# Kernel tuning notes

Measured on AMD Instinct MI355X. Metric: run time of the kernel, lower is better.

Reference implementation:

```python
import jax, jax.numpy as jnp
import numpy as np

EPS = 1e-8  # torch F.cosine_similarity eps


def setup_inputs() -> dict:
    key = jax.random.key(0)
    k1, k2 = jax.random.split(key)
    B, D = 8192, 512
    return {
        "label_tensor": jnp.arange(B, dtype=jnp.int64),
        "feature_a": jax.random.normal(k1, (B, D), dtype=jnp.float32),
        "feature_b": jax.random.normal(k2, (B, D), dtype=jnp.float32),
        "affine_w": jnp.ones((1,), dtype=jnp.float32),   # AffineModel scale
        "affine_b": jnp.zeros((1,), dtype=jnp.float32),  # AffineModel bias
    }


def reference(label_tensor, feature_a, feature_b, affine_w, affine_b):
    # cos_score[i, j] = cos(a_i, b_j): normalize then one [B,D]x[D,B] GEMM
    a_n = feature_a / jnp.maximum(
        jnp.linalg.norm(feature_a, axis=1, keepdims=True), EPS)
    b_n = feature_b / jnp.maximum(
        jnp.linalg.norm(feature_b, axis=1, keepdims=True), EPS)
    cos_score = jnp.einsum("id,jd->ij", a_n, b_n)  # [B, B]
    cos_score = affine_w[0] * cos_score + affine_b[0]  # AffineModel
    # cross-entropy with labels = arange(B) -> diagonal of log_softmax
    logp = jax.nn.log_softmax(cos_score, axis=1)
    B = cos_score.shape[0]
    loss = -jnp.mean(logp[jnp.arange(B), jnp.arange(B)])
    return (loss, cos_score)
```

## Files before the change

### kernel.cpp

```cpp
#include <hip/hip_runtime.h>
#include <hip/hip_bf16.h>

#define B_ROWS 8192
#define DIM 512

typedef __bf16 bf16x8 __attribute__((ext_vector_type(8)));
typedef float f32x4 __attribute__((ext_vector_type(4)));

__device__ inline ushort f2bf(float x) {
    __hip_bfloat16 h = __float2bfloat16(x);
    return __builtin_bit_cast(ushort, h);
}

__global__ __launch_bounds__(256) void norm_kernel(const float* __restrict__ A,
                                                   const float* __restrict__ Bf,
                                                   ushort* __restrict__ An,
                                                   ushort* __restrict__ Bn) {
    int gw = (blockIdx.x * 256 + threadIdx.x) >> 6;
    int lane = threadIdx.x & 63;
    const float* src;
    ushort* dst;
    if (gw < B_ROWS) {
        src = A + (size_t)gw * DIM;
        dst = An + (size_t)gw * DIM;
    } else {
        src = Bf + (size_t)(gw - B_ROWS) * DIM;
        dst = Bn + (size_t)(gw - B_ROWS) * DIM;
    }
    const float4* s4 = (const float4*)src;
    float4 v0 = s4[lane * 2];
    float4 v1 = s4[lane * 2 + 1];
    float ss = v0.x * v0.x + v0.y * v0.y + v0.z * v0.z + v0.w * v0.w
             + v1.x * v1.x + v1.y * v1.y + v1.z * v1.z + v1.w * v1.w;
#pragma unroll
    for (int m = 32; m >= 1; m >>= 1) ss += __shfl_xor(ss, m, 64);
    float scale = 1.0f / fmaxf(sqrtf(ss), 1e-8f);
    union { ushort us[8]; uint4 q; } o;
    o.us[0] = f2bf(v0.x * scale); o.us[1] = f2bf(v0.y * scale);
    o.us[2] = f2bf(v0.z * scale); o.us[3] = f2bf(v0.w * scale);
    o.us[4] = f2bf(v1.x * scale); o.us[5] = f2bf(v1.y * scale);
    o.us[6] = f2bf(v1.z * scale); o.us[7] = f2bf(v1.w * scale);
    ((uint4*)dst)[lane] = o.q;
}

#define GLDS(src, dst) __builtin_amdgcn_global_load_lds( \
    (const __attribute__((address_space(1))) unsigned int*)(src), \
    (__attribute__((address_space(3))) unsigned int*)(dst), 16, 0, 0)

__global__ __launch_bounds__(512, 2) void gemm_kernel(
    const ushort* __restrict__ An, const ushort* __restrict__ Bn,
    float* __restrict__ C, float* __restrict__ rowpart,
    const float* __restrict__ wp, const float* __restrict__ bp) {
    __shared__ ushort ldsA[2][8192];
    __shared__ ushort ldsB[2][8192];

    const int t = threadIdx.x;
    const int brow = blockIdx.y * 256;
    const int bcol = blockIdx.x * 256;
    const int wid = t >> 6, lane = t & 63;
    const int wr = wid >> 2, wc = wid & 3;
    const int fr = lane & 15;
    const int fhi = lane >> 4;

    const int srow = t >> 2;
    const int schunk = (t & 3) ^ ((t >> 3) & 3);
    const ushort* gA0 = An + (size_t)(brow + srow) * DIM + schunk * 8;
    const ushort* gA1 = gA0 + (size_t)128 * DIM;
    const ushort* gB0 = Bn + (size_t)(bcol + srow) * DIM + schunk * 8;
    const ushort* gB1 = gB0 + (size_t)128 * DIM;

#define STAGE(buf, kt) do { const int k0_ = (kt) * 32;            \
        GLDS(gA0 + k0_, &ldsA[buf][t * 8]);                       \
        GLDS(gA1 + k0_, &ldsA[buf][4096 + t * 8]);                \
        GLDS(gB0 + k0_, &ldsB[buf][t * 8]);                       \
        GLDS(gB1 + k0_, &ldsB[buf][4096 + t * 8]); } while (0)

    f32x4 acc[8][4];
#pragma unroll
    for (int i = 0; i < 8; i++)
#pragma unroll
        for (int j = 0; j < 4; j++) acc[i][j] = (f32x4){0.f, 0.f, 0.f, 0.f};

    const int rchunk = (fhi ^ ((fr >> 1) & 3)) * 8;

    STAGE(0, 0);
    __syncthreads();

    int cur = 0;
#pragma unroll
    for (int kt = 0; kt < 16; ++kt) {
        if (kt < 15) STAGE(cur ^ 1, kt + 1);
        bf16x8 af[8], bfr[4];
#pragma unroll
        for (int m = 0; m < 8; ++m)
            af[m] = *(const bf16x8*)&ldsA[cur][(wr * 128 + m * 16 + fr) * 32 + rchunk];
#pragma unroll
        for (int n = 0; n < 4; ++n)
            bfr[n] = *(const bf16x8*)&ldsB[cur][(wc * 64 + n * 16 + fr) * 32 + rchunk];
        __builtin_amdgcn_s_setprio(1);
#pragma unroll
        for (int m = 0; m < 8; ++m)
#pragma unroll
            for (int n = 0; n < 4; ++n)
                acc[m][n] = __builtin_amdgcn_mfma_f32_16x16x32_bf16(af[m], bfr[n], acc[m][n], 0, 0, 0);
        __builtin_amdgcn_s_setprio(0);
        __syncthreads();
        cur ^= 1;
    }

    const float w = wp[0], bb = bp[0];
    const float M = fabsf(w) + fabsf(bb);
    float* part = (float*)&ldsA[0][0];
#pragma unroll
    for (int m = 0; m < 8; ++m) {
#pragma unroll
        for (int r = 0; r < 4; ++r) {
            const int rloc = wr * 128 + m * 16 + fhi * 4 + r;
            const size_t grow = (size_t)(brow + rloc);
            float psum = 0.f;
#pragma unroll
            for (int n = 0; n < 4; ++n) {
                const int gcol = bcol + wc * 64 + n * 16 + fr;
                float s = fmaf(w, acc[m][n][r], bb);
                C[grow * B_ROWS + gcol] = s;
                psum += __expf(s - M);
            }
#pragma unroll
            for (int msk = 1; msk <= 8; msk <<= 1) psum += __shfl_xor(psum, msk, 64);
            if (fr == 0) part[wc * 256 + rloc] = psum;
        }
    }
    __syncthreads();
    if (t < 256) {
        float s = part[t] + part[256 + t] + part[512 + t] + part[768 + t];
        rowpart[(size_t)blockIdx.x * B_ROWS + brow + t] = s;
    }
#undef STAGE
}

__global__ __launch_bounds__(256) void loss_kernel(const float* __restrict__ C,
                                                   const float* __restrict__ rowpart,
                                                   const float* __restrict__ wp,
                                                   const float* __restrict__ bp,
                                                   float* __restrict__ out0) {
    __shared__ float sred[4];
    const int row = blockIdx.x * 256 + threadIdx.x;
    float rs = 0.f;
#pragma unroll
    for (int j = 0; j < 32; ++j) rs += rowpart[(size_t)j * B_ROWS + row];
    const float M = fabsf(wp[0]) + fabsf(bp[0]);
    const float sii = C[(size_t)row * B_ROWS + row];
    float v = sii - M - __logf(rs);
#pragma unroll
    for (int msk = 32; msk >= 1; msk >>= 1) v += __shfl_xor(v, msk, 64);
    if ((threadIdx.x & 63) == 0) sred[threadIdx.x >> 6] = v;
    __syncthreads();
    if (threadIdx.x == 0) {
        float tot = sred[0] + sred[1] + sred[2] + sred[3];
        atomicAdd(out0, -tot / (float)B_ROWS);
    }
}

extern "C" void kernel_launch(void* const* d_in, const int* in_sizes, int n_in,
                              void* d_out, int out_size, void* d_ws, size_t ws_size,
                              hipStream_t stream) {
    const float* A  = (const float*)d_in[1];
    const float* Bf = (const float*)d_in[2];
    const float* wp = (const float*)d_in[3];
    const float* bp = (const float*)d_in[4];
    float* out = (float*)d_out;

    ushort* An = (ushort*)d_ws;
    ushort* Bn = An + (size_t)B_ROWS * DIM;
    float* rowpart = (float*)((char*)d_ws + (size_t)2 * B_ROWS * DIM * sizeof(ushort));

    hipMemsetAsync(d_out, 0, sizeof(float), stream);
    norm_kernel<<<dim3(16384 * 64 / 256), 256, 0, stream>>>(A, Bf, An, Bn);
    dim3 grid(B_ROWS / 256, B_ROWS / 256);
    gemm_kernel<<<grid, 512, 0, stream>>>(An, Bn, out + 1, rowpart, wp, bp);
    loss_kernel<<<B_ROWS / 256, 256, 0, stream>>>(out + 1, rowpart, wp, bp, out);
}
```

Before: 397.7 us.

## Restructure GEMM main loop into K=64 steps with interleaved staging and MFMA quadrants

The GEMM kernel now stages a K=64 slice per iteration (8 iterations instead of 16) and splits each iteration into four MFMA quadrants. Global-to-LDS loads for A and B halves are interleaved between quadrants under explicit s_waitcnt vmcnt and s_barrier control. The aim is to overlap memory staging with tensor-core work and halve the per-K-step barrier count. In exchange it doubles LDS use to 128 KB per block, which may cut occupancy below the two blocks per CU requested by the launch bounds. The hand-placed barriers and vmcnt counts also risk subtle ordering errors.

Result: faster. 387.7 us (-2.5%).

```diff
diff --git a/kernel.cpp b/kernel.cpp
--- a/kernel.cpp
+++ b/kernel.cpp
@@ -47,12 +47,18 @@
     (const __attribute__((address_space(1))) unsigned int*)(src), \
     (__attribute__((address_space(3))) unsigned int*)(dst), 16, 0, 0)
 
+#define STG(bufv, ab, PTR, doff, ktv) do {                                   \
+    GLDS((PTR) + (ktv) * 64,      L + (((bufv)*2 + (ab))*2 + 0)*8192 + (doff)); \
+    GLDS((PTR) + (ktv) * 64 + 32, L + (((bufv)*2 + (ab))*2 + 1)*8192 + (doff)); } while (0)
+
+#define BARRIER() asm volatile("s_barrier" ::: "memory")
+
 __global__ __launch_bounds__(512, 2) void gemm_kernel(
     const ushort* __restrict__ An, const ushort* __restrict__ Bn,
     float* __restrict__ C, float* __restrict__ rowpart,
     const float* __restrict__ wp, const float* __restrict__ bp) {
-    __shared__ ushort ldsA[2][8192];
-    __shared__ ushort ldsB[2][8192];
+    __shared__ ushort lds[2][2][2][8192];
+    ushort* L = &lds[0][0][0][0];
 
     const int t = threadIdx.x;
     const int brow = blockIdx.y * 256;
@@ -62,18 +68,19 @@
     const int fr = lane & 15;
     const int fhi = lane >> 4;
 
-    const int srow = t >> 2;
-    const int schunk = (t & 3) ^ ((t >> 3) & 3);
-    const ushort* gA0 = An + (size_t)(brow + srow) * DIM + schunk * 8;
-    const ushort* gA1 = gA0 + (size_t)128 * DIM;
-    const ushort* gB0 = Bn + (size_t)(bcol + srow) * DIM + schunk * 8;
-    const ushort* gB1 = gB0 + (size_t)128 * DIM;
-
-#define STAGE(buf, kt) do { const int k0_ = (kt) * 32;            \
-        GLDS(gA0 + k0_, &ldsA[buf][t * 8]);                       \
-        GLDS(gA1 + k0_, &ldsA[buf][4096 + t * 8]);                \
-        GLDS(gB0 + k0_, &ldsB[buf][t * 8]);                       \
-        GLDS(gB1 + k0_, &ldsB[buf][4096 + t * 8]); } while (0)
+    const int schunk8 = ((t & 3) ^ ((t >> 3) & 3)) * 8;
+    const int srowAa = (t >> 8) * 128 + ((t >> 2) & 63);
+    const int srowBa = (t >> 7) * 64 + ((t >> 2) & 31);
+    const ushort* pAa = An + (size_t)(brow + srowAa) * DIM + schunk8;
+    const ushort* pAb = An + (size_t)(brow + srowAa + 64) * DIM + schunk8;
+    const ushort* pBa = Bn + (size_t)(bcol + srowBa) * DIM + schunk8;
+    const ushort* pBb = Bn + (size_t)(bcol + srowBa + 32) * DIM + schunk8;
+    const int dAa = t * 8 + (t >> 8) * 2048;
+    const int dAb = dAa + 2048;
+    const int dBa = t * 8 + (t >> 7) * 1024;
+    const int dBb = dBa + 1024;
+
+    const int rchunk8 = (fhi ^ ((fr >> 1) & 3)) * 8;
 
     f32x4 acc[8][4];
 #pragma unroll
@@ -81,36 +88,76 @@
 #pragma unroll
         for (int j = 0; j < 4; j++) acc[i][j] = (f32x4){0.f, 0.f, 0.f, 0.f};
 
-    const int rchunk = (fhi ^ ((fr >> 1) & 3)) * 8;
-
-    STAGE(0, 0);
+    bf16x8 af[4][2], b0[2][2], b1[2][2];
+
+    auto rdA = [&](int buf, int mb) {
+#pragma unroll
+        for (int i = 0; i < 4; ++i)
+#pragma unroll
+            for (int kk = 0; kk < 2; ++kk)
+                af[i][kk] = *(const bf16x8*)(L + ((buf * 2 + 0) * 2 + kk) * 8192
+                            + (wr * 128 + (mb + i) * 16 + fr) * 32 + rchunk8);
+    };
+    auto rdB = [&](bf16x8 (&b)[2][2], int buf, int nb) {
+#pragma unroll
+        for (int j = 0; j < 2; ++j)
+#pragma unroll
+            for (int kk = 0; kk < 2; ++kk)
+                b[j][kk] = *(const bf16x8*)(L + ((buf * 2 + 1) * 2 + kk) * 8192
+                           + (wc * 64 + (nb + j) * 16 + fr) * 32 + rchunk8);
+    };
+    auto mfma16 = [&](bf16x8 (&b)[2][2], int mb, int nb) {
+        __builtin_amdgcn_sched_barrier(0);
+        __builtin_amdgcn_s_setprio(1);
+#pragma unroll
+        for (int i = 0; i < 4; ++i)
+#pragma unroll
+            for (int j = 0; j < 2; ++j)
+#pragma unroll
+                for (int kk = 0; kk < 2; ++kk)
+                    acc[mb + i][nb + j] = __builtin_amdgcn_mfma_f32_16x16x32_bf16(
+                        af[i][kk], b[j][kk], acc[mb + i][nb + j], 0, 0, 0);
+        __builtin_amdgcn_s_setprio(0);
+        __builtin_amdgcn_sched_barrier(0);
+    };
+
+    STG(0, 0, pAa, dAa, 0);
+    STG(0, 1, pBa, dBa, 0);
+    STG(0, 0, pAb, dAb, 0);
+    STG(0, 1, pBb, dBb, 0);
+    asm volatile("s_waitcnt vmcnt(0)\n\ts_barrier" ::: "memory");
+
+#pragma unroll
+    for (int kt = 0; kt < 8; ++kt) {
+        const int cur = kt & 1, nxt = cur ^ 1;
+        if (kt < 7) STG(nxt, 0, pAa, dAa, kt + 1);
+        rdA(cur, 0);
+        rdB(b0, cur, 0);
+        BARRIER();
+        mfma16(b0, 0, 0);
+        if (kt == 7) { asm volatile("s_waitcnt vmcnt(0)\n\ts_barrier" ::: "memory"); }
+        else         { asm volatile("s_waitcnt vmcnt(2)\n\ts_barrier" ::: "memory"); }
+        if (kt < 7) STG(nxt, 1, pBa, dBa, kt + 1);
+        rdB(b1, cur, 2);
+        BARRIER();
+        mfma16(b1, 0, 2);
+        BARRIER();
+        if (kt < 7) STG(nxt, 0, pAb, dAb, kt + 1);
+        rdA(cur, 4);
+        BARRIER();
+        mfma16(b1, 4, 2);
+        BARRIER();
+        if (kt < 7) STG(nxt, 1, pBb, dBb, kt + 1);
+        BARRIER();
+        mfma16(b0, 4, 0);
+        if (kt < 7) { asm volatile("s_waitcnt vmcnt(4)\n\ts_barrier" ::: "memory"); }
+        else        { BARRIER(); }
+    }
+
     __syncthreads();
-
-    int cur = 0;
-#pragma unroll
-    for (int kt = 0; kt < 16; ++kt) {
-        if (kt < 15) STAGE(cur ^ 1, kt + 1);
-        bf16x8 af[8], bfr[4];
-#pragma unroll
-        for (int m = 0; m < 8; ++m)
-            af[m] = *(const bf16x8*)&ldsA[cur][(wr * 128 + m * 16 + fr) * 32 + rchunk];
-#pragma unroll
-        for (int n = 0; n < 4; ++n)
-            bfr[n] = *(const bf16x8*)&ldsB[cur][(wc * 64 + n * 16 + fr) * 32 + rchunk];
-        __builtin_amdgcn_s_setprio(1);
-#pragma unroll
-        for (int m = 0; m < 8; ++m)
-#pragma unroll
-            for (int n = 0; n < 4; ++n)
-                acc[m][n] = __builtin_amdgcn_mfma_f32_16x16x32_bf16(af[m], bfr[n], acc[m][n], 0, 0, 0);
-        __builtin_amdgcn_s_setprio(0);
-        __syncthreads();
-        cur ^= 1;
-    }
-
     const float w = wp[0], bb = bp[0];
     const float M = fabsf(w) + fabsf(bb);
-    float* part = (float*)&ldsA[0][0];
+    float* part = (float*)L;
 #pragma unroll
     for (int m = 0; m < 8; ++m) {
 #pragma unroll
@@ -135,7 +182,6 @@
         float s = part[t] + part[256 + t] + part[512 + t] + part[768 + t];
         rowpart[(size_t)blockIdx.x * B_ROWS + brow + t] = s;
     }
-#undef STAGE
 }
 
 __global__ __launch_bounds__(256) void loss_kernel(const float* __restrict__ C,
```
